# Kernel tuning notes

Measured on AMD Instinct MI355X. Metric: run time of the kernel, lower is better.

The kernel has to match this reference:

```python
import jax, jax.numpy as jnp
import numpy as np

L, D_MODEL, D_INNER, D_STATE, NHEADS, HEADDIM, D_CONV, D_INT, NCLS = 4, 256, 512, 16, 8, 64, 4, 256, 10
IN_FEAT, T_LEN, BATCH = 64, 1024, 8
D_IN_PROJ = 2 * D_INNER + 2 * D_STATE + NHEADS  # 1064
CONV_DIM = D_INNER + 2 * D_STATE  # 544
EPS = 1e-5


def silu(x):
    return x * jax.nn.sigmoid(x)


def layernorm(x, w, b):
    mu = jnp.mean(x, -1, keepdims=True)
    xc = x - mu
    var = jnp.mean(xc * xc, -1, keepdims=True)
    return xc * jax.lax.rsqrt(var + EPS) * w + b


def depthwise_causal_conv(x, w, b):
    # x: (B,T,C), w: (C,K), b: (C,) ; torch Conv1d(groups=C, padding=K-1)[..., :T]
    K = w.shape[1]
    T = x.shape[1]
    xp = jnp.pad(x, ((0, 0), (K - 1, 0), (0, 0)))
    acc = b
    for k in range(K):
        acc = acc + xp[:, k:k + T, :] * w[:, k]
    return acc


def ssm_scan(xh, dt, A, Bm, Cm):
    # xh: (B,T,H,P), dt: (B,T,H), A: (H,), Bm/Cm: (B,T,N) (ngroups=1)
    B_, T, H, P = xh.shape
    N = Bm.shape[-1]

    def step(h, inp):
        dt_t, x_t, B_t, C_t = inp  # (B,H),(B,H,P),(B,N),(B,N)
        dA = jnp.exp(dt_t * A)  # (B,H)
        h = h * dA[..., None, None] + (dt_t[..., None] * x_t)[..., None] * B_t[:, None, None, :]
        y = jnp.einsum('bhpn,bn->bhp', h, C_t)
        return h, y

    h0 = jnp.zeros((B_, H, P, N), xh.dtype)
    xs_t = (dt.transpose(1, 0, 2), xh.transpose(1, 0, 2, 3), Bm.transpose(1, 0, 2), Cm.transpose(1, 0, 2))
    _, ys = jax.lax.scan(step, h0, xs_t)
    return ys.transpose(1, 0, 2, 3)  # (B,T,H,P)


def mamba2_mixer(x, in_proj_w, conv_w, conv_b, dt_bias, A_log, D, ssm_norm_w, out_proj_w):
    B_, T, _ = x.shape
    zxbcdt = x @ in_proj_w.T  # (B,T,D_IN_PROJ)
    z = zxbcdt[..., :D_INNER]
    xBC = zxbcdt[..., D_INNER:D_INNER + CONV_DIM]
    dt = jax.nn.softplus(zxbcdt[..., -NHEADS:] + dt_bias)
    xBC = silu(depthwise_causal_conv(xBC, conv_w, conv_b))
    xs = xBC[..., :D_INNER]
    Bm = xBC[..., D_INNER:D_INNER + D_STATE]
    Cm = xBC[..., D_INNER + D_STATE:]
    A = -jnp.exp(A_log)  # (H,)
    xh = xs.reshape(B_, T, NHEADS, HEADDIM)
    y = ssm_scan(xh, dt, A, Bm, Cm) + D[:, None] * xh
    y = y.reshape(B_, T, D_INNER)
    # RMSNormGated (norm_before_gate=False): rmsnorm(y * silu(z)) * weight
    y = y * silu(z)
    y = y * jax.lax.rsqrt(jnp.mean(y * y, -1, keepdims=True) + EPS) * ssm_norm_w
    return y @ out_proj_w.T


def _forward(x, input_proj_w, input_proj_b, norm1_w, norm1_b, in_proj_w, conv_w, conv_b,
             dt_bias, A_log, D, ssm_norm_w, out_proj_w, norm2_w, norm2_b,
             fc1_w, fc1_b, fc2_w, fc2_b, normf_w, normf_b, fc_w, fc_b):
    h = jnp.swapaxes(x, 1, 2) @ input_proj_w.T + input_proj_b  # (B,T,d_model)
    residual = None
    for i in range(L):
        flip = (i % 2 == 1)
        if flip:
            h = h[:, ::-1]
            residual = residual[:, ::-1] if residual is not None else None
        residual = h + residual if residual is not None else h
        hn = layernorm(residual, norm1_w[i], norm1_b[i])
        hm = mamba2_mixer(hn, in_proj_w[i], conv_w[i], conv_b[i], dt_bias[i], A_log[i],
                          D[i], ssm_norm_w[i], out_proj_w[i])
        residual = hm + residual
        hn2 = layernorm(residual, norm2_w[i], norm2_b[i])
        yy = hn2 @ fc1_w[i].T + fc1_b[i]
        y1, gate = jnp.split(yy, 2, axis=-1)
        h = (y1 * silu(gate)) @ fc2_w[i].T + fc2_b[i]
        if flip:
            h = h[:, ::-1]
            residual = residual[:, ::-1]
    residual = h + residual
    out = layernorm(residual, normf_w, normf_b)
    out = jnp.mean(out, axis=1)  # mean over time
    return out @ fc_w.T + fc_b  # (B, n_classes)


def setup_inputs() -> dict:
    key = jax.random.key(0)
    ks = jax.random.split(key, 12)
    n = lambda k, shp, s=0.02: jax.random.normal(k, shp, jnp.float32) * s
    return {
        'x': jax.random.normal(ks[0], (BATCH, IN_FEAT, T_LEN), jnp.float32),
        'input_proj_w': n(ks[1], (D_MODEL, IN_FEAT)),
        'input_proj_b': jnp.zeros((D_MODEL,), jnp.float32),
        'norm1_w': jnp.ones((L, D_MODEL), jnp.float32),
        'norm1_b': jnp.zeros((L, D_MODEL), jnp.float32),
        'in_proj_w': n(ks[2], (L, D_IN_PROJ, D_MODEL)),
        'conv_w': n(ks[3], (L, CONV_DIM, D_CONV), 0.2),
        'conv_b': jnp.zeros((L, CONV_DIM), jnp.float32),
        'dt_bias': jnp.log(jnp.expm1(jax.random.uniform(ks[4], (L, NHEADS), jnp.float32, 0.001, 0.1))),
        'A_log': jnp.log(jax.random.uniform(ks[5], (L, NHEADS), jnp.float32, 1.0, 16.0)),
        'D': jnp.ones((L, NHEADS), jnp.float32),
        'ssm_norm_w': jnp.ones((L, D_INNER), jnp.float32),
        'out_proj_w': n(ks[6], (L, D_MODEL, D_INNER)),
        'norm2_w': jnp.ones((L, D_MODEL), jnp.float32),
        'norm2_b': jnp.zeros((L, D_MODEL), jnp.float32),
        'fc1_w': n(ks[7], (L, 2 * D_INT, D_MODEL)),
        'fc1_b': jnp.zeros((L, 2 * D_INT), jnp.float32),
        'fc2_w': n(ks[8], (L, D_MODEL, D_INT)),
        'fc2_b': jnp.zeros((L, D_MODEL), jnp.float32),
        'normf_w': jnp.ones((D_MODEL,), jnp.float32),
        'normf_b': jnp.zeros((D_MODEL,), jnp.float32),
        'fc_w': n(ks[9], (NCLS, D_MODEL)),
        'fc_b': jnp.zeros((NCLS,), jnp.float32),
    }


def reference(x, input_proj_w, input_proj_b, norm1_w, norm1_b, in_proj_w, conv_w, conv_b,
              dt_bias, A_log, D, ssm_norm_w, out_proj_w, norm2_w, norm2_b,
              fc1_w, fc1_b, fc2_w, fc2_b, normf_w, normf_b, fc_w, fc_b):
    return _forward(x, input_proj_w, input_proj_b, norm1_w, norm1_b, in_proj_w, conv_w, conv_b,
                    dt_bias, A_log, D, ssm_norm_w, out_proj_w, norm2_w, norm2_b,
                    fc1_w, fc1_b, fc2_w, fc2_b, normf_w, normf_b, fc_w, fc_b)
```

## Files before the change

### kernel.cpp

```cpp
#include <hip/hip_runtime.h>
#include <math.h>

#define NLAYERS   4
#define D_MODEL   256
#define D_INNER   512
#define D_STATE   16
#define NHEADS    8
#define HEADDIM   64
#define D_CONV    4
#define D_INT     256
#define NCLS      10
#define IN_FEAT   64
#define T_LEN     1024
#define BATCH     8
#define D_IN_PROJ 1064
#define CONV_DIM  544
#define EPS       1e-5f
#define NTOK      (BATCH*T_LEN)
#define QCH       32
#define NCH       (T_LEN/QCH)

typedef __attribute__((ext_vector_type(8))) short bf16x8;
typedef __attribute__((ext_vector_type(4))) float f32x4;

__device__ __forceinline__ float silu_f(float x) { return x / (1.f + expf(-x)); }
__device__ __forceinline__ float softplus_f(float x) { return x > 20.f ? x : log1pf(expf(x)); }

typedef __attribute__((address_space(3))) void       lds_void_t;
typedef __attribute__((address_space(1))) const void gbl_void_t;
__device__ __forceinline__ void gload16(void* lds, const void* g) {
    __builtin_amdgcn_global_load_lds((gbl_void_t*)g, (lds_void_t*)lds, 16, 0, 0);
}

__device__ __forceinline__ unsigned short f2bf(float f) {
    unsigned u = __float_as_uint(f);
    return (unsigned short)((u + 0x7fffu + ((u >> 16) & 1u)) >> 16);
}
__device__ __forceinline__ float bf2f(unsigned short h) {
    return __uint_as_float((unsigned)h << 16);
}
__device__ __forceinline__ ushort2 split2(float f) {
    unsigned short hi = f2bf(f);
    unsigned short lo = f2bf(f - bf2f(hi));
    return make_ushort2(hi, lo);
}

template<int NW>
__device__ __forceinline__ float block_sum(float v, float* red) {
#pragma unroll
    for (int off = 32; off > 0; off >>= 1) v += __shfl_down(v, off, 64);
    int lane = threadIdx.x & 63, wid = threadIdx.x >> 6;
    __syncthreads();
    if (lane == 0) red[wid] = v;
    __syncthreads();
    float s = 0.f;
#pragma unroll
    for (int i = 0; i < NW; ++i) s += red[i];
    return s;
}

__global__ __launch_bounds__(256) void pack_split_kernel(
    const float* __restrict__ src, unsigned short* __restrict__ hi,
    unsigned short* __restrict__ lo, int n4)
{
    int i = blockIdx.x * 256 + threadIdx.x;
    if (i >= n4) return;
    float4 v = ((const float4*)src)[i];
    ushort2 a = split2(v.x), b = split2(v.y), c = split2(v.z), d = split2(v.w);
    ((ushort4*)hi)[i] = make_ushort4(a.x, b.x, c.x, d.x);
    ((ushort4*)lo)[i] = make_ushort4(a.y, b.y, c.y, d.y);
}

__global__ __launch_bounds__(256) void pack_fc1_kernel(
    const float* __restrict__ src, unsigned short* __restrict__ hi,
    unsigned short* __restrict__ lo, int n4)
{
    int i4 = blockIdx.x * 256 + threadIdx.x;
    if (i4 >= n4) return;
    int gl  = i4 / (512 * 64);
    int rem = i4 % (512 * 64);
    int r   = rem / 64;
    int k4  = rem % 64;
    int x = r >> 6, ii = r & 63;
    int orig = (ii < 32) ? (x * 32 + ii) : (256 + x * 32 + (ii - 32));
    float4 v = ((const float4*)src)[(gl * 512 + orig) * 64 + k4];
    ushort2 a = split2(v.x), b = split2(v.y), c = split2(v.z), d = split2(v.w);
    ((ushort4*)hi)[i4] = make_ushort4(a.x, b.x, c.x, d.x);
    ((ushort4*)lo)[i4] = make_ushort4(a.y, b.y, c.y, d.y);
}

__global__ __launch_bounds__(256) void input_proj_kernel(
    const float* __restrict__ x, const float* __restrict__ w,
    const float* __restrict__ bias, float* __restrict__ h)
{
    int bt = blockIdx.x;
    int b = bt / T_LEN, t = bt % T_LEN;
    __shared__ float xs[IN_FEAT];
    int tid = threadIdx.x;
    if (tid < IN_FEAT) xs[tid] = x[(b * IN_FEAT + tid) * T_LEN + t];
    __syncthreads();
    float acc = bias[tid];
    const float4* wr = (const float4*)(w + tid * IN_FEAT);
#pragma unroll 4
    for (int f4 = 0; f4 < IN_FEAT / 4; ++f4) {
        float4 wv = wr[f4];
        acc += xs[f4 * 4 + 0] * wv.x + xs[f4 * 4 + 1] * wv.y +
               xs[f4 * 4 + 2] * wv.z + xs[f4 * 4 + 3] * wv.w;
    }
    h[bt * D_MODEL + tid] = acc;
}

__global__ __launch_bounds__(256) void add_ln_kernel(
    const float* __restrict__ a, const float* __restrict__ b,
    float* __restrict__ sum_out, unsigned short* __restrict__ hi,
    unsigned short* __restrict__ lo, float* __restrict__ f32out,
    const float* __restrict__ w, const float* __restrict__ bias)
{
    __shared__ float red[4];
    int row = blockIdx.x, d = threadIdx.x;
    size_t o = (size_t)row * D_MODEL + d;
    float v = a[o];
    if (b) v += b[o];
    if (sum_out) sum_out[o] = v;
    float mean = block_sum<4>(v, red) * (1.f / D_MODEL);
    float xc = v - mean;
    float var = block_sum<4>(xc * xc, red) * (1.f / D_MODEL);
    float r = xc * rsqrtf(var + EPS) * w[d] + bias[d];
    if (hi) { ushort2 s = split2(r); hi[o] = s.x; lo[o] = s.y; }
    if (f32out) f32out[o] = r;
}

template<int BM>
__global__ __launch_bounds__(128) void gemm_mfma(
    const unsigned short* __restrict__ Ahi, const unsigned short* __restrict__ Alo,
    const unsigned short* __restrict__ Whi, const unsigned short* __restrict__ Wlo,
    const float* __restrict__ bias, const float* __restrict__ resid,
    float* __restrict__ C, int N, int K)
{
    constexpr int MFRAG   = BM / 32;
    constexpr int AROUNDS = BM / 32;
    __shared__ unsigned short sAh[BM * 32], sAl[BM * 32];
    __shared__ unsigned short sBh[64 * 32], sBl[64 * 32];
    const int tid = threadIdx.x;
    const int lane = tid & 63, wm = tid >> 6;
    const int m0 = blockIdx.y * BM, n0 = blockIdx.x * 64;

    const int srow = tid >> 2;
    const int sk   = (tid & 3) * 8;
    const unsigned short* gAh = Ahi + (size_t)(m0 + srow) * K + sk;
    const unsigned short* gAl = Alo + (size_t)(m0 + srow) * K + sk;
    int bn  = n0 + srow;      if (bn  > N - 1) bn  = N - 1;
    int bn2 = n0 + 32 + srow; if (bn2 > N - 1) bn2 = N - 1;
    const unsigned short* gBh  = Whi + (size_t)bn  * K + sk;
    const unsigned short* gBh2 = Whi + (size_t)bn2 * K + sk;
    const unsigned short* gBl  = Wlo + (size_t)bn  * K + sk;
    const unsigned short* gBl2 = Wlo + (size_t)bn2 * K + sk;
    const size_t rK32 = (size_t)32 * K;

    const int fr = lane & 15, kg = lane >> 4;
    const int abase = (wm * (BM / 2) + fr) * 32 + kg * 8;
    const int bbase = fr * 32 + kg * 8;

    f32x4 acc[MFRAG][4] = {};

    for (int k0 = 0; k0 < K; k0 += 32) {
#pragma unroll
        for (int rr = 0; rr < AROUNDS; ++rr) {
            gload16(&sAh[tid * 8 + rr * 1024], gAh + (size_t)rr * rK32);
            gload16(&sAl[tid * 8 + rr * 1024], gAl + (size_t)rr * rK32);
        }
        gload16(&sBh[tid * 8],        gBh);
        gload16(&sBh[tid * 8 + 1024], gBh2);
        gload16(&sBl[tid * 8],        gBl);
        gload16(&sBl[tid * 8 + 1024], gBl2);
        gAh += 32; gAl += 32; gBh += 32; gBh2 += 32; gBl += 32; gBl2 += 32;
        __syncthreads();

        bf16x8 ah[MFRAG], al[MFRAG], bh[4], bl[4];
#pragma unroll
        for (int fm = 0; fm < MFRAG; ++fm) {
            ah[fm] = *(const bf16x8*)&sAh[abase + fm * 512];
            al[fm] = *(const bf16x8*)&sAl[abase + fm * 512];
        }
#pragma unroll
        for (int fn = 0; fn < 4; ++fn) {
            bh[fn] = *(const bf16x8*)&sBh[bbase + fn * 512];
            bl[fn] = *(const bf16x8*)&sBl[bbase + fn * 512];
        }
#pragma unroll
        for (int fm = 0; fm < MFRAG; ++fm)
#pragma unroll
            for (int fn = 0; fn < 4; ++fn) {
                acc[fm][fn] = __builtin_amdgcn_mfma_f32_16x16x32_bf16(ah[fm], bh[fn], acc[fm][fn], 0, 0, 0);
                acc[fm][fn] = __builtin_amdgcn_mfma_f32_16x16x32_bf16(ah[fm], bl[fn], acc[fm][fn], 0, 0, 0);
                acc[fm][fn] = __builtin_amdgcn_mfma_f32_16x16x32_bf16(al[fm], bh[fn], acc[fm][fn], 0, 0, 0);
            }
        __syncthreads();
    }

    const int orow0 = kg * 4;
#pragma unroll
    for (int fm = 0; fm < MFRAG; ++fm)
#pragma unroll
        for (int fn = 0; fn < 4; ++fn) {
            int n = n0 + fn * 16 + fr;
            if (n < N) {
                float bv = bias ? bias[n] : 0.f;
#pragma unroll
                for (int r = 0; r < 4; ++r) {
                    int m = m0 + wm * (BM / 2) + fm * 16 + orow0 + r;
                    size_t off = (size_t)m * N + n;
                    float v = acc[fm][fn][r] + bv;
                    if (resid) v += resid[off];
                    C[off] = v;
                }
            }
        }
}

__global__ __launch_bounds__(128) void gemm_mfma_glu(
    const unsigned short* __restrict__ Ahi, const unsigned short* __restrict__ Alo,
    const unsigned short* __restrict__ Whi, const unsigned short* __restrict__ Wlo,
    const float* __restrict__ bias,
    unsigned short* __restrict__ Ghi, unsigned short* __restrict__ Glo, int K)
{
    constexpr int BM = 64;
    __shared__ unsigned short sAh[BM * 32], sAl[BM * 32];
    __shared__ unsigned short sBh[64 * 32], sBl[64 * 32];
    const int tid = threadIdx.x;
    const int lane = tid & 63, wm = tid >> 6;
    const int m0 = blockIdx.y * BM, n0 = blockIdx.x * 64;

    const int srow = tid >> 2;
    const int sk   = (tid & 3) * 8;
    const unsigned short* gAh = Ahi + (size_t)(m0 + srow) * K + sk;
    const unsigned short* gAl = Alo + (size_t)(m0 + srow) * K + sk;
    const unsigned short* gBh  = Whi + (size_t)(n0 + srow) * K + sk;
    const unsigned short* gBh2 = Whi + (size_t)(n0 + 32 + srow) * K + sk;
    const unsigned short* gBl  = Wlo + (size_t)(n0 + srow) * K + sk;
    const unsigned short* gBl2 = Wlo + (size_t)(n0 + 32 + srow) * K + sk;
    const size_t rK32 = (size_t)32 * K;

    const int fr = lane & 15, kg = lane >> 4;
    const int abase = (wm * 32 + fr) * 32 + kg * 8;
    const int bbase = fr * 32 + kg * 8;

    f32x4 acc[2][4] = {};

    for (int k0 = 0; k0 < K; k0 += 32) {
#pragma unroll
        for (int rr = 0; rr < 2; ++rr) {
            gload16(&sAh[tid * 8 + rr * 1024], gAh + (size_t)rr * rK32);
            gload16(&sAl[tid * 8 + rr * 1024], gAl + (size_t)rr * rK32);
        }
        gload16(&sBh[tid * 8],        gBh);
        gload16(&sBh[tid * 8 + 1024], gBh2);
        gload16(&sBl[tid * 8],        gBl);
        gload16(&sBl[tid * 8 + 1024], gBl2);
        gAh += 32; gAl += 32; gBh += 32; gBh2 += 32; gBl += 32; gBl2 += 32;
        __syncthreads();

        bf16x8 ah[2], al[2], bh[4], bl[4];
#pragma unroll
        for (int fm = 0; fm < 2; ++fm) {
            ah[fm] = *(const bf16x8*)&sAh[abase + fm * 512];
            al[fm] = *(const bf16x8*)&sAl[abase + fm * 512];
        }
#pragma unroll
        for (int fn = 0; fn < 4; ++fn) {
            bh[fn] = *(const bf16x8*)&sBh[bbase + fn * 512];
            bl[fn] = *(const bf16x8*)&sBl[bbase + fn * 512];
        }
#pragma unroll
        for (int fm = 0; fm < 2; ++fm)
#pragma unroll
            for (int fn = 0; fn < 4; ++fn) {
                acc[fm][fn] = __builtin_amdgcn_mfma_f32_16x16x32_bf16(ah[fm], bh[fn], acc[fm][fn], 0, 0, 0);
                acc[fm][fn] = __builtin_amdgcn_mfma_f32_16x16x32_bf16(ah[fm], bl[fn], acc[fm][fn], 0, 0, 0);
                acc[fm][fn] = __builtin_amdgcn_mfma_f32_16x16x32_bf16(al[fm], bh[fn], acc[fm][fn], 0, 0, 0);
            }
        __syncthreads();
    }

    const int orow0 = kg * 4;
#pragma unroll
    for (int fm = 0; fm < 2; ++fm)
#pragma unroll
        for (int fn = 0; fn < 2; ++fn) {
            int lc = (n0 >> 1) + fn * 16 + fr;
            float by = bias[lc], bg = bias[256 + lc];
#pragma unroll
            for (int r = 0; r < 4; ++r) {
                int m = m0 + wm * 32 + fm * 16 + orow0 + r;
                float y1 = acc[fm][fn][r] + by;
                float gt = acc[fm][fn + 2][r] + bg;
                float g  = y1 * silu_f(gt);
                ushort2 s = split2(g);
                size_t off = (size_t)m * D_INT + lc;
                Ghi[off] = s.x; Glo[off] = s.y;
            }
        }
}

__global__ __launch_bounds__(256) void conv_dt_kernel(
    const float* __restrict__ zx, const float* __restrict__ cw,
    const float* __restrict__ cb, const float* __restrict__ dt_bias,
    const float* __restrict__ A_log, float* __restrict__ out,
    float2* __restrict__ dtda, int dir)
{
    const int NCG = CONV_DIM / 4;
    int idx = blockIdx.x * 256 + threadIdx.x;
    if (idx < NTOK * NCG) {
        int cg = idx % NCG;
        int bt = idx / NCG;
        int c = cg * 4;
        int s = bt % T_LEN, b = bt / T_LEN;
        float4 acc = *(const float4*)(cb + c);
        float4 w0 = *(const float4*)(cw + (c + 0) * 4);
        float4 w1 = *(const float4*)(cw + (c + 1) * 4);
        float4 w2 = *(const float4*)(cw + (c + 2) * 4);
        float4 w3 = *(const float4*)(cw + (c + 3) * 4);
#pragma unroll
        for (int k = 0; k < D_CONV; ++k) {
            int sj = s + k - (D_CONV - 1);
            if (sj >= 0) {
                int t = dir ? (T_LEN - 1 - sj) : sj;
                float4 xv = *(const float4*)(zx + ((size_t)(b * T_LEN + t)) * D_IN_PROJ + D_INNER + c);
                acc.x += xv.x * (&w0.x)[k];
                acc.y += xv.y * (&w1.x)[k];
                acc.z += xv.z * (&w2.x)[k];
                acc.w += xv.w * (&w3.x)[k];
            }
        }
        int tout = dir ? (T_LEN - 1 - s) : s;
        float4 r = make_float4(silu_f(acc.x), silu_f(acc.y), silu_f(acc.z), silu_f(acc.w));
        *(float4*)(out + ((size_t)(b * T_LEN + tout)) * CONV_DIM + c) = r;
    } else {
        int j = idx - NTOK * NCG;
        if (j < NTOK * NHEADS) {
            int bt = j >> 3, h = j & 7;
            float dtraw = zx[(size_t)bt * D_IN_PROJ + (D_IN_PROJ - NHEADS) + h] + dt_bias[h];
            float dt = softplus_f(dtraw);
            float Ac = -expf(A_log[h]);
            dtda[(size_t)bt * NHEADS + h] = make_float2(dt, expf(dt * Ac));
        }
    }
}

__global__ __launch_bounds__(64) void scan_local_kernel(
    const float2* __restrict__ dtda, const float* __restrict__ xbc,
    const float* __restrict__ Dvec, float* __restrict__ y,
    float* __restrict__ hend, float* __restrict__ pf, int dir)
{
    __shared__ float  sx[QCH][HEADDIM];
    __shared__ float  sBC[QCH][32];
    __shared__ float2 sd[QCH];
    int bx = blockIdx.x;
    int c = bx & (NCH - 1), h = (bx >> 5) & 7, b = bx >> 8;
    int p = threadIdx.x;
    int s0 = c * QCH;
#pragma unroll
    for (int i = 0; i < 8; ++i) {
        int idx = i * 64 + p;
        int si = idx >> 4, l4 = (idx & 15) * 4;
        int s = s0 + si; int t = dir ? (T_LEN - 1 - s) : s;
        size_t row = (size_t)b * T_LEN + t;
        *(float4*)&sx[si][l4] = *(const float4*)(xbc + row * CONV_DIM + h * HEADDIM + l4);
    }
#pragma unroll
    for (int i = 0; i < 4; ++i) {
        int idx = i * 64 + p;
        int si = idx >> 3, l4 = (idx & 7) * 4;
        int s = s0 + si; int t = dir ? (T_LEN - 1 - s) : s;
        size_t row = (size_t)b * T_LEN + t;
        *(float4*)&sBC[si][l4] = *(const float4*)(xbc + row * CONV_DIM + D_INNER + l4);
    }
    if (p < QCH) {
        int s = s0 + p; int t = dir ? (T_LEN - 1 - s) : s;
        sd[p] = dtda[((size_t)b * T_LEN + t) * NHEADS + h];
    }
    __syncthreads();
    float Dh = Dvec[h];
    float hreg[16];
#pragma unroll
    for (int n = 0; n < 16; ++n) hreg[n] = 0.f;
    float pp = 1.f;
    for (int si = 0; si < QCH; ++si) {
        float2 dd = sd[si];
        float xv = sx[si][p];
        float dtx = dd.x * xv;
        float Bv[16], Cv[16];
#pragma unroll
        for (int j = 0; j < 4; ++j) {
            float4 t4 = *(const float4*)&sBC[si][j * 4];
            Bv[j*4+0] = t4.x; Bv[j*4+1] = t4.y; Bv[j*4+2] = t4.z; Bv[j*4+3] = t4.w;
            float4 u4 = *(const float4*)&sBC[si][16 + j * 4];
            Cv[j*4+0] = u4.x; Cv[j*4+1] = u4.y; Cv[j*4+2] = u4.z; Cv[j*4+3] = u4.w;
        }
#pragma unroll
        for (int n = 0; n < 16; ++n) hreg[n] = fmaf(hreg[n], dd.y, dtx * Bv[n]);
        float yv = Dh * xv;
#pragma unroll
        for (int n = 0; n < 16; ++n) yv = fmaf(hreg[n], Cv[n], yv);
        pp *= dd.y;
        int s = s0 + si; int t = dir ? (T_LEN - 1 - s) : s;
        y[((size_t)b * T_LEN + t) * D_INNER + h * HEADDIM + p] = yv;
        if (p == 0) pf[((size_t)(b * NHEADS + h)) * T_LEN + s] = pp;
    }
    float4* he = (float4*)(hend + ((size_t)((b * NHEADS + h) * NCH + c)) * 1024 + p * 16);
#pragma unroll
    for (int j = 0; j < 4; ++j)
        he[j] = make_float4(hreg[j*4+0], hreg[j*4+1], hreg[j*4+2], hreg[j*4+3]);
}

__global__ __launch_bounds__(256) void scan_combine_kernel(
    const float* __restrict__ hend, const float* __restrict__ pf,
    float* __restrict__ hin_out)
{
    int e = blockIdx.x * 256 + threadIdx.x;
    int base = e >> 10, tid = e & 1023;
    float hin = 0.f;
    for (int c = 0; c < NCH; ++c) {
        hin_out[((size_t)base * NCH + c) * 1024 + tid] = hin;
        float Pc = pf[(size_t)base * T_LEN + c * QCH + (QCH - 1)];
        hin = hend[((size_t)base * NCH + c) * 1024 + tid] + Pc * hin;
    }
}

__global__ __launch_bounds__(64) void scan_fix_kernel(
    const float* __restrict__ hin_in, const float* __restrict__ pf,
    const float* __restrict__ xbc, float* __restrict__ y, int dir)
{
    __shared__ float sC[QCH][16];
    __shared__ float spf[QCH];
    int c = 1 + (blockIdx.x % (NCH - 1));
    int bh = blockIdx.x / (NCH - 1);
    int b = bh >> 3, h = bh & 7;
    int p = threadIdx.x;
    size_t base = (size_t)bh;
    int s0 = c * QCH;
    float hin[16];
    {
        const float4* hp = (const float4*)(hin_in + (base * NCH + c) * 1024 + p * 16);
#pragma unroll
        for (int j = 0; j < 4; ++j) {
            float4 v = hp[j];
            hin[j*4+0] = v.x; hin[j*4+1] = v.y; hin[j*4+2] = v.z; hin[j*4+3] = v.w;
        }
    }
#pragma unroll
    for (int i = 0; i < 2; ++i) {
        int idx = i * 64 + p;
        int si = idx >> 2, l4 = (idx & 3) * 4;
        int s = s0 + si; int t = dir ? (T_LEN - 1 - s) : s;
        size_t row = (size_t)b * T_LEN + t;
        *(float4*)&sC[si][l4] = *(const float4*)(xbc + row * CONV_DIM + D_INNER + D_STATE + l4);
    }
    if (p < QCH) spf[p] = pf[base * T_LEN + s0 + p];
    __syncthreads();
    for (int si = 0; si < QCH; ++si) {
        float Cv[16];
#pragma unroll
        for (int j = 0; j < 4; ++j) {
            float4 u4 = *(const float4*)&sC[si][j * 4];
            Cv[j*4+0] = u4.x; Cv[j*4+1] = u4.y; Cv[j*4+2] = u4.z; Cv[j*4+3] = u4.w;
        }
        float yv = 0.f;
#pragma unroll
        for (int n = 0; n < 16; ++n) yv = fmaf(hin[n], Cv[n], yv);
        int s = s0 + si; int t = dir ? (T_LEN - 1 - s) : s;
        float* yp = y + ((size_t)b * T_LEN + t) * D_INNER + h * HEADDIM + p;
        *yp += spf[si] * yv;
    }
}

__global__ __launch_bounds__(512) void gated_rms_kernel(
    const float* __restrict__ y, const float* __restrict__ zx,
    const float* __restrict__ w, unsigned short* __restrict__ hi,
    unsigned short* __restrict__ lo)
{
    __shared__ float red[8];
    int row = blockIdx.x, d = threadIdx.x;
    float z = zx[(size_t)row * D_IN_PROJ + d];
    float v = y[(size_t)row * D_INNER + d] * silu_f(z);
    float ss = block_sum<8>(v * v, red);
    float r = rsqrtf(ss * (1.f / D_INNER) + EPS);
    float o = v * r * w[d];
    ushort2 s = split2(o);
    size_t off = (size_t)row * D_INNER + d;
    hi[off] = s.x; lo[off] = s.y;
}

__global__ void zero_mean_kernel(float* mean) {
    int i = blockIdx.x * 256 + threadIdx.x;
    if (i < BATCH * D_MODEL) mean[i] = 0.f;
}
__global__ __launch_bounds__(256) void mean_kernel(
    const float* __restrict__ hn, float* __restrict__ mean)
{
    int b = blockIdx.x >> 4;
    int slab = blockIdx.x & 15;
    int d = threadIdx.x;
    float s = 0.f;
    int t0 = slab * 64;
    for (int t = t0; t < t0 + 64; ++t) s += hn[((size_t)(b * T_LEN + t)) * D_MODEL + d];
    atomicAdd(&mean[b * D_MODEL + d], s * (1.f / T_LEN));
}
__global__ void logits_kernel(const float* __restrict__ mean,
                              const float* __restrict__ fcw,
                              const float* __restrict__ fcb,
                              float* __restrict__ out)
{
    int tid = threadIdx.x;
    if (tid < BATCH * NCLS) {
        int b = tid / NCLS, c = tid % NCLS;
        float s = fcb[c];
        for (int d = 0; d < D_MODEL; ++d) s += mean[b * D_MODEL + d] * fcw[c * D_MODEL + d];
        out[tid] = s;
    }
}

extern "C" void kernel_launch(void* const* d_in, const int* in_sizes, int n_in,
                              void* d_out, int out_size, void* d_ws, size_t ws_size,
                              hipStream_t stream)
{
    const float* x            = (const float*)d_in[0];
    const float* input_proj_w = (const float*)d_in[1];
    const float* input_proj_b = (const float*)d_in[2];
    const float* norm1_w      = (const float*)d_in[3];
    const float* norm1_b      = (const float*)d_in[4];
    const float* in_proj_w    = (const float*)d_in[5];
    const float* conv_w       = (const float*)d_in[6];
    const float* conv_b       = (const float*)d_in[7];
    const float* dt_bias      = (const float*)d_in[8];
    const float* A_log        = (const float*)d_in[9];
    const float* Dvec         = (const float*)d_in[10];
    const float* ssm_norm_w   = (const float*)d_in[11];
    const float* out_proj_w   = (const float*)d_in[12];
    const float* norm2_w      = (const float*)d_in[13];
    const float* norm2_b      = (const float*)d_in[14];
    const float* fc1_w        = (const float*)d_in[15];
    const float* fc1_b        = (const float*)d_in[16];
    const float* fc2_w        = (const float*)d_in[17];
    const float* fc2_b        = (const float*)d_in[18];
    const float* normf_w      = (const float*)d_in[19];
    const float* normf_b      = (const float*)d_in[20];
    const float* fc_w         = (const float*)d_in[21];
    const float* fc_b         = (const float*)d_in[22];
    float* out = (float*)d_out;

    char* ws = (char*)d_ws;
    float*          RES  = (float*)(ws + 0);
    float*          H    = (float*)(ws + 8388608);
    unsigned short* HNh  = (unsigned short*)(ws + 16777216);
    unsigned short* HNl  = (unsigned short*)(ws + 20971520);
    float*          ZX   = (float*)(ws + 25165824);
    float*          XBCC = (float*)(ws + 60030976);
    float*          YSSM = (float*)(ws + 77856768);
    unsigned short* YSh  = (unsigned short*)(ws + 94633984);
    unsigned short* YSl  = (unsigned short*)(ws + 103022592);
    unsigned short* GLh  = (unsigned short*)(ws + 111411200);
    unsigned short* GLl  = (unsigned short*)(ws + 115605504);
    unsigned short* WIH  = (unsigned short*)(ws + 119799808);
    unsigned short* WIL  = (unsigned short*)(ws + 121978880);
    unsigned short* WOH  = (unsigned short*)(ws + 124157952);
    unsigned short* WOL  = (unsigned short*)(ws + 125206528);
    unsigned short* W1H  = (unsigned short*)(ws + 126255104);
    unsigned short* W1L  = (unsigned short*)(ws + 127303680);
    unsigned short* W2H  = (unsigned short*)(ws + 128352256);
    unsigned short* W2L  = (unsigned short*)(ws + 128876544);
    float2*         DTDA = (float2*)(ws + 129400832);
    float*          MEAN = (float*)(ws + 129925120);
    float*          HNF  = XBCC;
    float*          PF   = (float*)(ws + 16777216);
    float*          HEND = (float*)(ws + 111411200);
    float*          HIN  = (float*)(ws + 94633984);

    pack_split_kernel<<<1064, 256, 0, stream>>>(in_proj_w,  WIH, WIL, NLAYERS * D_IN_PROJ * D_MODEL / 4);
    pack_split_kernel<<<512,  256, 0, stream>>>(out_proj_w, WOH, WOL, NLAYERS * D_MODEL * D_INNER / 4);
    pack_fc1_kernel  <<<512,  256, 0, stream>>>(fc1_w,      W1H, W1L, NLAYERS * 2 * D_INT * D_MODEL / 4);
    pack_split_kernel<<<256,  256, 0, stream>>>(fc2_w,      W2H, W2L, NLAYERS * D_MODEL * D_INT / 4);

    input_proj_kernel<<<NTOK, 256, 0, stream>>>(x, input_proj_w, input_proj_b, H);

    for (int i = 0; i < NLAYERS; ++i) {
        int dir = i & 1;
        add_ln_kernel<<<NTOK, 256, 0, stream>>>(
            H, i ? RES : nullptr, RES, HNh, HNl, nullptr,
            norm1_w + i * D_MODEL, norm1_b + i * D_MODEL);
        {
            dim3 g((D_IN_PROJ + 63) / 64, NTOK / 128);
            gemm_mfma<128><<<g, 128, 0, stream>>>(
                HNh, HNl, WIH + (size_t)i * D_IN_PROJ * D_MODEL, WIL + (size_t)i * D_IN_PROJ * D_MODEL,
                nullptr, nullptr, ZX, D_IN_PROJ, D_MODEL);
        }
        conv_dt_kernel<<<(NTOK * (CONV_DIM / 4) + NTOK * NHEADS + 255) / 256, 256, 0, stream>>>(
            ZX, conv_w + (size_t)i * CONV_DIM * D_CONV, conv_b + i * CONV_DIM,
            dt_bias + i * NHEADS, A_log + i * NHEADS, XBCC, DTDA, dir);
        scan_local_kernel<<<BATCH * NHEADS * NCH, 64, 0, stream>>>(
            DTDA, XBCC, Dvec + i * NHEADS, YSSM, HEND, PF, dir);
        scan_combine_kernel<<<BATCH * NHEADS * 1024 / 256, 256, 0, stream>>>(HEND, PF, HIN);
        scan_fix_kernel<<<BATCH * NHEADS * (NCH - 1), 64, 0, stream>>>(
            HIN, PF, XBCC, YSSM, dir);
        gated_rms_kernel<<<NTOK, 512, 0, stream>>>(YSSM, ZX, ssm_norm_w + i * D_INNER, YSh, YSl);
        {
            dim3 g(D_MODEL / 64, NTOK / 64);
            gemm_mfma<64><<<g, 128, 0, stream>>>(
                YSh, YSl, WOH + (size_t)i * D_MODEL * D_INNER, WOL + (size_t)i * D_MODEL * D_INNER,
                nullptr, RES, RES, D_MODEL, D_INNER);
        }
        add_ln_kernel<<<NTOK, 256, 0, stream>>>(
            RES, nullptr, nullptr, HNh, HNl, nullptr,
            norm2_w + i * D_MODEL, norm2_b + i * D_MODEL);
        {
            dim3 g((2 * D_INT) / 64, NTOK / 64);
            gemm_mfma_glu<<<g, 128, 0, stream>>>(
                HNh, HNl, W1H + (size_t)i * 2 * D_INT * D_MODEL, W1L + (size_t)i * 2 * D_INT * D_MODEL,
                fc1_b + i * 2 * D_INT, GLh, GLl, D_MODEL);
        }
        {
            dim3 g(D_MODEL / 64, NTOK / 64);
            gemm_mfma<64><<<g, 128, 0, stream>>>(
                GLh, GLl, W2H + (size_t)i * D_MODEL * D_INT, W2L + (size_t)i * D_MODEL * D_INT,
                fc2_b + i * D_MODEL, nullptr, H, D_MODEL, D_INT);
        }
    }

    add_ln_kernel<<<NTOK, 256, 0, stream>>>(
        H, RES, nullptr, nullptr, nullptr, HNF, normf_w, normf_b);
    zero_mean_kernel<<<(BATCH * D_MODEL + 255) / 256, 256, 0, stream>>>(MEAN);
    mean_kernel<<<BATCH * 16, 256, 0, stream>>>(HNF, MEAN);
    logits_kernel<<<1, 128, 0, stream>>>(MEAN, fc_w, fc_b, out);
}
```

Baseline: 866.7 us.

## Tile input projection over time and XOR-swizzle GEMM shared-memory layout

The input projection kernel now handles 16 timesteps per block. It loads each thread's weight row into registers once and reads the input tile with coalesced float4 loads, so it no longer reloads weights and does strided scalar reads for every token. Separately, both MFMA GEMM kernels apply an XOR swizzle on the k-group when writing and reading shared memory, to avoid LDS bank conflicts. The trade-offs are more register pressure in the projection kernel and extra index arithmetic in the GEMMs.

```diff
diff --git a/kernel.cpp b/kernel.cpp
--- a/kernel.cpp
+++ b/kernel.cpp
@@ -89,25 +89,41 @@
     ((ushort4*)lo)[i4] = make_ushort4(a.y, b.y, c.y, d.y);
 }
 
+#define TT 16
 __global__ __launch_bounds__(256) void input_proj_kernel(
     const float* __restrict__ x, const float* __restrict__ w,
     const float* __restrict__ bias, float* __restrict__ h)
 {
-    int bt = blockIdx.x;
-    int b = bt / T_LEN, t = bt % T_LEN;
-    __shared__ float xs[IN_FEAT];
+    __shared__ float xs[TT][IN_FEAT + 4];
+    int blk = blockIdx.x;
+    int b = blk / (T_LEN / TT), tc = blk % (T_LEN / TT);
+    int t0 = tc * TT;
     int tid = threadIdx.x;
-    if (tid < IN_FEAT) xs[tid] = x[(b * IN_FEAT + tid) * T_LEN + t];
+    {
+        int f = tid >> 2, j = tid & 3;
+        float4 v = *(const float4*)(x + ((size_t)(b * IN_FEAT + f)) * T_LEN + t0 + j * 4);
+        xs[j * 4 + 0][f] = v.x;
+        xs[j * 4 + 1][f] = v.y;
+        xs[j * 4 + 2][f] = v.z;
+        xs[j * 4 + 3][f] = v.w;
+    }
     __syncthreads();
-    float acc = bias[tid];
-    const float4* wr = (const float4*)(w + tid * IN_FEAT);
-#pragma unroll 4
-    for (int f4 = 0; f4 < IN_FEAT / 4; ++f4) {
-        float4 wv = wr[f4];
-        acc += xs[f4 * 4 + 0] * wv.x + xs[f4 * 4 + 1] * wv.y +
-               xs[f4 * 4 + 2] * wv.z + xs[f4 * 4 + 3] * wv.w;
-    }
-    h[bt * D_MODEL + tid] = acc;
+    int d = tid;
+    float4 wr[16];
+    const float4* wp = (const float4*)(w + d * IN_FEAT);
+#pragma unroll
+    for (int i = 0; i < 16; ++i) wr[i] = wp[i];
+    float bv = bias[d];
+#pragma unroll
+    for (int t = 0; t < TT; ++t) {
+        float acc = bv;
+#pragma unroll
+        for (int i = 0; i < 16; ++i) {
+            float4 xv = *(const float4*)&xs[t][i * 4];
+            acc += xv.x * wr[i].x + xv.y * wr[i].y + xv.z * wr[i].z + xv.w * wr[i].w;
+        }
+        h[((size_t)(b * T_LEN + t0 + t)) * D_MODEL + d] = acc;
+    }
 }
 
 __global__ __launch_bounds__(256) void add_ln_kernel(
@@ -146,7 +162,7 @@
     const int m0 = blockIdx.y * BM, n0 = blockIdx.x * 64;
 
     const int srow = tid >> 2;
-    const int sk   = (tid & 3) * 8;
+    const int sk   = (((tid & 3) ^ ((srow >> 1) & 3)) * 8);
     const unsigned short* gAh = Ahi + (size_t)(m0 + srow) * K + sk;
     const unsigned short* gAl = Alo + (size_t)(m0 + srow) * K + sk;
     int bn  = n0 + srow;      if (bn  > N - 1) bn  = N - 1;
@@ -158,8 +174,9 @@
     const size_t rK32 = (size_t)32 * K;
 
     const int fr = lane & 15, kg = lane >> 4;
-    const int abase = (wm * (BM / 2) + fr) * 32 + kg * 8;
-    const int bbase = fr * 32 + kg * 8;
+    const int kgs = kg ^ ((fr >> 1) & 3);
+    const int abase = (wm * (BM / 2) + fr) * 32 + kgs * 8;
+    const int bbase = fr * 32 + kgs * 8;
 
     f32x4 acc[MFRAG][4] = {};
 
@@ -232,7 +249,7 @@
     const int m0 = blockIdx.y * BM, n0 = blockIdx.x * 64;
 
     const int srow = tid >> 2;
-    const int sk   = (tid & 3) * 8;
+    const int sk   = (((tid & 3) ^ ((srow >> 1) & 3)) * 8);
     const unsigned short* gAh = Ahi + (size_t)(m0 + srow) * K + sk;
     const unsigned short* gAl = Alo + (size_t)(m0 + srow) * K + sk;
     const unsigned short* gBh  = Whi + (size_t)(n0 + srow) * K + sk;
@@ -242,8 +259,9 @@
     const size_t rK32 = (size_t)32 * K;
 
     const int fr = lane & 15, kg = lane >> 4;
-    const int abase = (wm * 32 + fr) * 32 + kg * 8;
-    const int bbase = fr * 32 + kg * 8;
+    const int kgs = kg ^ ((fr >> 1) & 3);
+    const int abase = (wm * 32 + fr) * 32 + kgs * 8;
+    const int bbase = fr * 32 + kgs * 8;
 
     f32x4 acc[2][4] = {};
 
@@ -581,7 +599,7 @@
     pack_fc1_kernel  <<<512,  256, 0, stream>>>(fc1_w,      W1H, W1L, NLAYERS * 2 * D_INT * D_MODEL / 4);
     pack_split_kernel<<<256,  256, 0, stream>>>(fc2_w,      W2H, W2L, NLAYERS * D_MODEL * D_INT / 4);
 
-    input_proj_kernel<<<NTOK, 256, 0, stream>>>(x, input_proj_w, input_proj_b, H);
+    input_proj_kernel<<<BATCH * (T_LEN / TT), 256, 0, stream>>>(x, input_proj_w, input_proj_b, H);
 
     for (int i = 0; i < NLAYERS; ++i) {
         int dir = i & 1;
```

Result: faster. 820.8 us (-5.3%).
